# Kernel tuning notes

Hardware: AMD Instinct MI355X
Metric: run time of the kernel (lower is better)

The kernel has to match this reference:

```python
import jax, jax.numpy as jnp
import numpy as np

Q, A, R, S, K = 256, 28, 512, 256, 2  # n_quantize, n_aux, n_resch, n_skipch, kernel_size
DEPTH, REPEAT = 10, 3
L = DEPTH * REPEAT  # 30 layers
T = 8192


def setup_inputs() -> dict:
    key = jax.random.key(0)
    ks = jax.random.split(key, 24)
    w = lambda k, shape: jax.random.normal(k, shape, dtype=jnp.float32) * 0.05
    return {
        "x": jax.random.randint(ks[0], (1, T), 0, Q, dtype=jnp.int32),
        "h": jax.random.normal(ks[1], (1, A, T), dtype=jnp.float32),
        "Wc": w(ks[2], (R, Q, K)), "bc": w(ks[3], (R,)),
        "Wds": w(ks[4], (L, R, R, K)), "bds": w(ks[5], (L, R)),
        "Wdt": w(ks[6], (L, R, R, K)), "bdt": w(ks[7], (L, R)),
        "Was": w(ks[8], (L, R, A, 1)), "bas": w(ks[9], (L, R)),
        "Wat": w(ks[10], (L, R, A, 1)), "bat": w(ks[11], (L, R)),
        "Wsk": w(ks[12], (L, S, R, 1)), "bsk": w(ks[13], (L, S)),
        "Wr": w(ks[14], (L, R, R, 1)), "br": w(ks[15], (L, R)),
        "Wp1": w(ks[16], (S, S, 1)), "bp1": w(ks[17], (S,)),
        "Wp2": w(ks[18], (Q, S, 1)), "bp2": w(ks[19], (Q,)),
    }


def _cconv(z, w, b, d):
    # causal dilated conv: z [1,C,T], w [O,C,K] -> [1,O,T]
    pad = (w.shape[2] - 1) * d
    y = jax.lax.conv_general_dilated(
        z, w, window_strides=(1,), padding=[(pad, 0)], rhs_dilation=(d,),
        dimension_numbers=("NCH", "OIH", "NCH"))
    return y + b[None, :, None]


def reference(x, h, Wc, bc, Wds, bds, Wdt, bdt, Was, bas, Wat, bat,
              Wsk, bsk, Wr, br, Wp1, bp1, Wp2, bp2):
    dilations = [2 ** i for i in range(DEPTH)] * REPEAT
    oh = jax.nn.one_hot(x, Q, dtype=Wc.dtype).transpose(0, 2, 1)  # [1,Q,T]
    out = _cconv(oh, Wc, bc, 1)  # [1,R,T]
    skip_sum = jnp.zeros((1, S, oh.shape[2]), dtype=Wc.dtype)
    for l, d in enumerate(dilations):
        s = _cconv(out, Wds[l], bds[l], d) + _cconv(h, Was[l], bas[l], 1)
        t = _cconv(out, Wdt[l], bdt[l], d) + _cconv(h, Wat[l], bat[l], 1)
        g = jax.nn.sigmoid(s) * jnp.tanh(t)  # gated activation
        skip_sum = skip_sum + _cconv(g, Wsk[l], bsk[l], 1)
        out = _cconv(g, Wr[l], br[l], 1) + out  # residual
    o = jax.nn.relu(skip_sum)
    o = jax.nn.relu(_cconv(o, Wp1, bp1, 1))
    o = _cconv(o, Wp2, bp2, 1)  # [1,Q,T]
    return o[0].T  # [T,Q], matches squeeze(0).transpose(0,1)
```

## Files before the change

kernel.cpp:

```cpp
#include <hip/hip_runtime.h>
#include <hip/hip_bf16.h>
#include <math.h>
#include <stdint.h>

#define T_LEN 8192
#define RCH   512
#define SCH   256
#define QCH   256
#define ACH   28
#define NLAYER 30
#define KGATE 1088
#define KSR   512
#define KPOST 256

typedef _Float16 f16x8 __attribute__((ext_vector_type(8)));
typedef float    f32x4 __attribute__((ext_vector_type(4)));

#define SB0() __builtin_amdgcn_sched_barrier(0)

static __device__ __forceinline__ unsigned short f2h(float v) {
    _Float16 h = (_Float16)v;
    return *reinterpret_cast<unsigned short*>(&h);
}

static __device__ __forceinline__ float fsig(float x) {
    return __builtin_amdgcn_rcpf(1.f + __expf(-x));
}

#define G2L(SRC, DST) __builtin_amdgcn_global_load_lds(                        \
    (__attribute__((address_space(1))) void*)(const void*)(SRC),              \
    (__attribute__((address_space(3))) void*)(void*)(DST), 16, 0, 0)

__global__ void pack_gate_v(const float* __restrict__ Wds,
                            const float* __restrict__ Wdt,
                            const float* __restrict__ Was,
                            const float* __restrict__ Wat,
                            unsigned short* __restrict__ dst) {
    int l = blockIdx.y;
    int c = blockIdx.x * 256 + threadIdx.x;
    int tile = c >> 6, lane = c & 63;
    int mt = tile / 34, kt = tile % 34;
    int m  = mt * 16 + (lane & 15);
    int k0 = kt * 32 + (lane >> 4) * 8;
    int br = m & 1, ch = m >> 1;
    const float* Wd = (br ? Wdt : Wds) + (size_t)l * RCH * RCH * 2;
    const float* Wa = (br ? Wat : Was) + (size_t)l * RCH * ACH;
    unsigned short o[8];
    if (k0 < 512) {
        const float* base = Wd + ((size_t)ch * 512 + k0) * 2;
        #pragma unroll
        for (int q = 0; q < 4; ++q) {
            float4 v = *(const float4*)(base + q * 4);
            o[q * 2 + 0] = f2h(v.x);
            o[q * 2 + 1] = f2h(v.z);
        }
    } else if (k0 < 1024) {
        const float* base = Wd + ((size_t)ch * 512 + (k0 - 512)) * 2;
        #pragma unroll
        for (int q = 0; q < 4; ++q) {
            float4 v = *(const float4*)(base + q * 4);
            o[q * 2 + 0] = f2h(v.y);
            o[q * 2 + 1] = f2h(v.w);
        }
    } else {
        int a0 = k0 - 1024;
        #pragma unroll
        for (int i = 0; i < 8; ++i)
            o[i] = (a0 + i < ACH) ? f2h(Wa[(size_t)ch * ACH + a0 + i]) : (unsigned short)0;
    }
    *(uint4*)&dst[(size_t)l * 1024 * KGATE + (size_t)tile * 512 + lane * 8] = *(uint4*)o;
}

__global__ void pack_sr_v(const float* __restrict__ Wsk,
                          const float* __restrict__ Wr,
                          unsigned short* __restrict__ dst) {
    int l = blockIdx.y;
    int c = blockIdx.x * 256 + threadIdx.x;
    int tile = c >> 6, lane = c & 63;
    int mt = tile >> 4, kt = tile & 15;
    int m  = mt * 16 + (lane & 15);
    int k0 = kt * 32 + (lane >> 4) * 8;
    const float* row = (m < SCH) ? (Wsk + (size_t)l * SCH * RCH + (size_t)m * 512)
                                 : (Wr  + (size_t)l * RCH * RCH + (size_t)(m - SCH) * 512);
    float4 v0 = *(const float4*)(row + k0);
    float4 v1 = *(const float4*)(row + k0 + 4);
    unsigned short o[8] = { f2h(v0.x), f2h(v0.y), f2h(v0.z), f2h(v0.w),
                            f2h(v1.x), f2h(v1.y), f2h(v1.z), f2h(v1.w) };
    *(uint4*)&dst[(size_t)l * 768 * KSR + (size_t)tile * 512 + lane * 8] = *(uint4*)o;
}

__global__ void pack_post_v(const float* __restrict__ W,
                            unsigned short* __restrict__ dst) {
    int c = blockIdx.x * 256 + threadIdx.x;
    int tile = c >> 6, lane = c & 63;
    int mt = tile >> 3, kt = tile & 7;
    int m  = mt * 16 + (lane & 15);
    int k0 = kt * 32 + (lane >> 4) * 8;
    float4 v0 = *(const float4*)(W + (size_t)m * 256 + k0);
    float4 v1 = *(const float4*)(W + (size_t)m * 256 + k0 + 4);
    unsigned short o[8] = { f2h(v0.x), f2h(v0.y), f2h(v0.z), f2h(v0.w),
                            f2h(v1.x), f2h(v1.y), f2h(v1.z), f2h(v1.w) };
    *(uint4*)&dst[(size_t)tile * 512 + lane * 8] = *(uint4*)o;
}

__global__ void transpose_wc(const float* __restrict__ Wc,
                             float* __restrict__ WcT) {
    int idx = blockIdx.x * 256 + threadIdx.x;
    int r = idx >> 9;
    int qt = idx & 511;
    int q = qt >> 1, tap = qt & 1;
    WcT[(size_t)q * 1024 + tap * 512 + r] = Wc[(size_t)r * 512 + qt];
}

__global__ void embed_v(const int* __restrict__ x,
                        const float* __restrict__ WcT,
                        const float* __restrict__ bc,
                        float* __restrict__ out_tm,
                        unsigned short* __restrict__ outhf) {
    int idx = blockIdx.x * 256 + threadIdx.x;
    int t = idx >> 6, rc = (idx & 63) * 8;
    int x1 = x[t];
    const float* w1 = WcT + (size_t)x1 * 1024 + 512 + rc;
    float4 a = *(const float4*)w1;
    float4 b = *(const float4*)(w1 + 4);
    float4 c0 = *(const float4*)(bc + rc);
    float4 c1 = *(const float4*)(bc + rc + 4);
    a.x += c0.x; a.y += c0.y; a.z += c0.z; a.w += c0.w;
    b.x += c1.x; b.y += c1.y; b.z += c1.z; b.w += c1.w;
    if (t > 0) {
        const float* w0 = WcT + (size_t)x[t - 1] * 1024 + rc;
        float4 d0 = *(const float4*)w0;
        float4 d1 = *(const float4*)(w0 + 4);
        a.x += d0.x; a.y += d0.y; a.z += d0.z; a.w += d0.w;
        b.x += d1.x; b.y += d1.y; b.z += d1.z; b.w += d1.w;
    }
    size_t o = (size_t)t * 512 + rc;
    *(float4*)&out_tm[o] = a;
    *(float4*)&out_tm[o + 4] = b;
    unsigned short p[8] = { f2h(a.x), f2h(a.y), f2h(a.z), f2h(a.w),
                            f2h(b.x), f2h(b.y), f2h(b.z), f2h(b.w) };
    *(uint4*)&outhf[o + 512 * 512] = *(uint4*)p;
}

__global__ void packh_kernel(const float* __restrict__ h,
                             unsigned short* __restrict__ h_tm) {
    int idx = blockIdx.x * 256 + threadIdx.x;
    int t = idx >> 6, a = idx & 63;
    h_tm[idx] = f2h(a < ACH ? h[(size_t)a * T_LEN + t] : 0.f);
}

__global__ void reluconv_v(const float* __restrict__ skip,
                           unsigned short* __restrict__ dst) {
    int idx = (blockIdx.x * 256 + threadIdx.x) * 8;
    float4 v0 = *(const float4*)(skip + idx);
    float4 v1 = *(const float4*)(skip + idx + 4);
    unsigned short o[8] = { f2h(fmaxf(v0.x, 0.f)), f2h(fmaxf(v0.y, 0.f)),
                            f2h(fmaxf(v0.z, 0.f)), f2h(fmaxf(v0.w, 0.f)),
                            f2h(fmaxf(v1.x, 0.f)), f2h(fmaxf(v1.y, 0.f)),
                            f2h(fmaxf(v1.z, 0.f)), f2h(fmaxf(v1.w, 0.f)) };
    *(uint4*)&dst[idx] = *(uint4*)o;
}

template<int MODE, int KT64, int MB>
__global__ __launch_bounds__(256) void mfma_gemm(
    const unsigned short* __restrict__ Apk,
    const unsigned short* __restrict__ B0,
    const unsigned short* __restrict__ B2,
    const float* __restrict__ bias0, const float* __restrict__ bias1,
    const float* __restrict__ bias2, const float* __restrict__ bias3,
    float* __restrict__ O0, float* __restrict__ O1,
    unsigned short* __restrict__ OB, int dil)
{
    constexpr int KT32 = KT64 * 2;
    constexpr int NWG = MB * 64;
    constexpr int CPX = NWG / 8;

    __shared__ unsigned short Bsm[2][128 * 64];

    const int tid  = threadIdx.x;
    const int lane = tid & 63, wave = tid >> 6;
    const int wm = wave & 1, wn = wave >> 1;

    const int bid = blockIdx.x;
    const int swz = (bid & 7) * CPX + (bid >> 3);
    const int mb  = swz % MB;
    const int tb  = swz / MB;
    const int m0  = mb * 128;
    const int t0  = tb * 128;

    const int kc   = ((lane & 7) ^ (lane >> 3)) * 8;
    const int rsub = lane >> 3;

    const size_t mt0 = (size_t)(mb * 8) + wm * 4;

    f32x4 acc[4][4];
    #pragma unroll
    for (int a = 0; a < 4; ++a)
        #pragma unroll
        for (int b = 0; b < 4; ++b) acc[a][b] = (f32x4){0.f, 0.f, 0.f, 0.f};

    f16x8 afrA[4][2], afrB[4][2], bfr[4][2];

    auto stage_tile = [&](int kt, int buf) {
        const int kb = kt * 64;
        #pragma unroll
        for (int j = 0; j < 4; ++j) {
            const int row = wave * 32 + j * 8 + rsub;
            const int tg  = t0 + row;
            const unsigned short* src;
            if constexpr (MODE == 0) {
                if (kb < 512)
                    src = B0 + (size_t)(512 + tg - dil) * 512 + kb + kc;
                else if (kb < 1024)
                    src = B0 + (size_t)(512 + tg) * 512 + (kb - 512) + kc;
                else
                    src = B2 + (size_t)tg * 64 + kc;
            } else if constexpr (MODE == 1) {
                src = B0 + (size_t)tg * 512 + kb + kc;
            } else {
                src = B0 + (size_t)tg * 256 + kb + kc;
            }
            G2L(src, &Bsm[buf][(wave * 4 + j) * 512]);
        }
    };

    auto load_afr = [&](int kt, f16x8 (&dst)[4][2]) {
        #pragma unroll
        for (int mi = 0; mi < 4; ++mi)
            #pragma unroll
            for (int ks = 0; ks < 2; ++ks)
                dst[mi][ks] = *(const f16x8*)(Apk +
                    ((mt0 + mi) * KT32 + (size_t)(kt * 2 + ks)) * 512 + lane * 8);
    };

    auto load_bfr = [&](int buf) {
        #pragma unroll
        for (int ni = 0; ni < 4; ++ni)
            #pragma unroll
            for (int ks = 0; ks < 2; ++ks) {
                const int trow = wn * 64 + ni * 16 + (lane & 15);
                const int kch  = ks * 4 + (lane >> 4);
                const int sch  = kch ^ (lane & 7);
                bfr[ni][ks] = *(const f16x8*)&Bsm[buf][trow * 64 + sch * 8];
            }
    };

    auto do_mfma = [&](f16x8 (&A)[4][2]) {
        #pragma unroll
        for (int mi = 0; mi < 4; ++mi)
            #pragma unroll
            for (int ni = 0; ni < 4; ++ni) {
                acc[mi][ni] = __builtin_amdgcn_mfma_f32_16x16x32_f16(
                    A[mi][0], bfr[ni][0], acc[mi][ni], 0, 0, 0);
                acc[mi][ni] = __builtin_amdgcn_mfma_f32_16x16x32_f16(
                    A[mi][1], bfr[ni][1], acc[mi][ni], 0, 0, 0);
            }
    };

    stage_tile(0, 0);
    SB0();
    load_afr(0, afrA);
    SB0();
    asm volatile("s_waitcnt vmcnt(8)" ::: "memory");
    SB0();
    __builtin_amdgcn_s_barrier();

    #pragma unroll
    for (int kt = 0; kt < KT64; ++kt) {
        const int cur = kt & 1;
        if (kt + 1 < KT64) {
            stage_tile(kt + 1, cur ^ 1);
            SB0();
            if (cur) load_afr(kt + 1, afrA);
            else     load_afr(kt + 1, afrB);
            SB0();
        }
        load_bfr(cur);
        if (cur) do_mfma(afrB);
        else     do_mfma(afrA);
        if (kt + 1 < KT64) {
            SB0();
            asm volatile("s_waitcnt vmcnt(8) lgkmcnt(0)" ::: "memory");
            SB0();
            __builtin_amdgcn_s_barrier();
        }
    }

    const int rb0 = (lane >> 4) * 4;
    #pragma unroll
    for (int mi = 0; mi < 4; ++mi) {
        #pragma unroll
        for (int ni = 0; ni < 4; ++ni) {
            int m = m0 + wm * 64 + mi * 16 + rb0;
            int t = t0 + wn * 64 + ni * 16 + (lane & 15);
            f32x4 v = acc[mi][ni];
            if constexpr (MODE == 0) {
                int c0 = m >> 1;
                float s0 = v.x + bias0[c0]     + bias2[c0];
                float tv0 = v.y + bias1[c0]     + bias3[c0];
                float s1 = v.z + bias0[c0 + 1] + bias2[c0 + 1];
                float tv1 = v.w + bias1[c0 + 1] + bias3[c0 + 1];
                float g0 = fsig(s0) * (2.f * fsig(2.f * tv0) - 1.f);
                float g1 = fsig(s1) * (2.f * fsig(2.f * tv1) - 1.f);
                unsigned int p = (unsigned int)f2h(g0) | ((unsigned int)f2h(g1) << 16);
                *(unsigned int*)&OB[(size_t)t * 512 + c0] = p;
            } else if constexpr (MODE == 1) {
                if (m < SCH) {
                    float4* p = (float4*)&O0[(size_t)t * 256 + m];
                    float4 o = *p;
                    o.x += v.x + bias0[m + 0];
                    o.y += v.y + bias0[m + 1];
                    o.z += v.z + bias0[m + 2];
                    o.w += v.w + bias0[m + 3];
                    *p = o;
                } else {
                    int c = m - SCH;
                    float4* p = (float4*)&O1[(size_t)t * 512 + c];
                    float4 o = *p;
                    o.x += v.x + bias1[c + 0];
                    o.y += v.y + bias1[c + 1];
                    o.z += v.z + bias1[c + 2];
                    o.w += v.w + bias1[c + 3];
                    *p = o;
                    uint2 pk;
                    pk.x = (unsigned int)f2h(o.x) | ((unsigned int)f2h(o.y) << 16);
                    pk.y = (unsigned int)f2h(o.z) | ((unsigned int)f2h(o.w) << 16);
                    *(uint2*)&OB[(size_t)(512 + t) * 512 + c] = pk;
                }
            } else if constexpr (MODE == 2) {
                float o0 = fmaxf(v.x + bias0[m + 0], 0.f);
                float o1 = fmaxf(v.y + bias0[m + 1], 0.f);
                float o2 = fmaxf(v.z + bias0[m + 2], 0.f);
                float o3 = fmaxf(v.w + bias0[m + 3], 0.f);
                uint2 pk;
                pk.x = (unsigned int)f2h(o0) | ((unsigned int)f2h(o1) << 16);
                pk.y = (unsigned int)f2h(o2) | ((unsigned int)f2h(o3) << 16);
                *(uint2*)&OB[(size_t)t * 256 + m] = pk;
            } else {
                float4 o;
                o.x = v.x + bias0[m + 0];
                o.y = v.y + bias0[m + 1];
                o.z = v.z + bias0[m + 2];
                o.w = v.w + bias0[m + 3];
                *(float4*)&O0[(size_t)t * 256 + m] = o;
            }
        }
    }
}

extern "C" void kernel_launch(void* const* d_in, const int* in_sizes, int n_in,
                              void* d_out, int out_size, void* d_ws, size_t ws_size,
                              hipStream_t stream) {
    const int*   x   = (const int*)  d_in[0];
    const float* h   = (const float*)d_in[1];
    const float* Wc  = (const float*)d_in[2];
    const float* bc  = (const float*)d_in[3];
    const float* Wds = (const float*)d_in[4];
    const float* bds = (const float*)d_in[5];
    const float* Wdt = (const float*)d_in[6];
    const float* bdt = (const float*)d_in[7];
    const float* Was = (const float*)d_in[8];
    const float* bas = (const float*)d_in[9];
    const float* Wat = (const float*)d_in[10];
    const float* bat = (const float*)d_in[11];
    const float* Wsk = (const float*)d_in[12];
    const float* bsk = (const float*)d_in[13];
    const float* Wr  = (const float*)d_in[14];
    const float* br  = (const float*)d_in[15];
    const float* Wp1 = (const float*)d_in[16];
    const float* bp1 = (const float*)d_in[17];
    const float* Wp2 = (const float*)d_in[18];
    const float* bp2 = (const float*)d_in[19];
    float* dout = (float*)d_out;

    const size_t WG_EL  = (size_t)1024 * KGATE;
    const size_t WSR_EL = (size_t)768 * KSR;
    char* w = (char*)d_ws;
    float*          out_tm = (float*)w;               w += (size_t)T_LEN * 512 * 4;
    unsigned short* outhf  = (unsigned short*)w;      w += (size_t)(T_LEN + 512) * 512 * 2;
    unsigned short* g_tm   = (unsigned short*)w;      w += (size_t)T_LEN * 512 * 2;
    unsigned short* h_tm   = (unsigned short*)w;      w += (size_t)T_LEN * 64 * 2;
    unsigned short* skiphf = (unsigned short*)w;      w += (size_t)T_LEN * 256 * 2;
    unsigned short* o1hf   = (unsigned short*)w;      w += (size_t)T_LEN * 256 * 2;
    unsigned short* Wp1_pk = (unsigned short*)w;      w += (size_t)256 * 256 * 2;
    unsigned short* Wp2_pk = (unsigned short*)w;      w += (size_t)256 * 256 * 2;
    float*          WcT    = (float*)w;               w += (size_t)QCH * 2 * RCH * 4;
    unsigned short* Wg_pk  = (unsigned short*)w;
    size_t used_base = (size_t)((char*)Wg_pk - (char*)d_ws);
    size_t need_bulk = used_base + (WG_EL + WSR_EL) * NLAYER * 2;
    const bool bulk = ws_size >= need_bulk;
    unsigned short* Wsr_pk = Wg_pk + (bulk ? WG_EL * NLAYER : WG_EL);
    float* skip = dout;

    hipMemsetAsync(skip, 0, (size_t)T_LEN * 256 * 4, stream);
    hipMemsetAsync(outhf, 0, (size_t)512 * 512 * 2, stream);

    transpose_wc<<<1024, 256, 0, stream>>>(Wc, WcT);
    embed_v<<<(T_LEN * 64) / 256, 256, 0, stream>>>(x, WcT, bc, out_tm, outhf);
    packh_kernel<<<(T_LEN * 64) / 256, 256, 0, stream>>>(h, h_tm);
    pack_post_v<<<32, 256, 0, stream>>>(Wp1, Wp1_pk);
    pack_post_v<<<32, 256, 0, stream>>>(Wp2, Wp2_pk);

    if (bulk) {
        pack_gate_v<<<dim3(544, NLAYER), 256, 0, stream>>>(Wds, Wdt, Was, Wat, Wg_pk);
        pack_sr_v<<<dim3(192, NLAYER), 256, 0, stream>>>(Wsk, Wr, Wsr_pk);
    }

    for (int l = 0; l < NLAYER; ++l) {
        int dil = 1 << (l % 10);
        const unsigned short* wg;
        const unsigned short* wsr;
        if (bulk) {
            wg  = Wg_pk  + (size_t)l * WG_EL;
            wsr = Wsr_pk + (size_t)l * WSR_EL;
        } else {
            pack_gate_v<<<dim3(544, 1), 256, 0, stream>>>(
                Wds + (size_t)l * RCH * RCH * 2, Wdt + (size_t)l * RCH * RCH * 2,
                Was + (size_t)l * RCH * ACH, Wat + (size_t)l * RCH * ACH, Wg_pk);
            pack_sr_v<<<dim3(192, 1), 256, 0, stream>>>(
                Wsk + (size_t)l * SCH * RCH, Wr + (size_t)l * RCH * RCH, Wsr_pk);
            wg = Wg_pk; wsr = Wsr_pk;
        }
        mfma_gemm<0, KGATE / 64, 8><<<512, 256, 0, stream>>>(
            wg, outhf, h_tm,
            bds + (size_t)l * RCH, bdt + (size_t)l * RCH,
            bas + (size_t)l * RCH, bat + (size_t)l * RCH,
            nullptr, nullptr, g_tm, dil);
        mfma_gemm<1, KSR / 64, 6><<<384, 256, 0, stream>>>(
            wsr, g_tm, nullptr,
            bsk + (size_t)l * SCH, br + (size_t)l * RCH, nullptr, nullptr,
            skip, out_tm, outhf, 0);
    }

    reluconv_v<<<(T_LEN * 256 / 8) / 256, 256, 0, stream>>>(skip, skiphf);
    mfma_gemm<2, KPOST / 64, 2><<<128, 256, 0, stream>>>(
        Wp1_pk, skiphf, nullptr, bp1, nullptr, nullptr, nullptr,
        nullptr, nullptr, o1hf, 0);
    mfma_gemm<3, KPOST / 64, 2><<<128, 256, 0, stream>>>(
        Wp2_pk, o1hf, nullptr, bp2, nullptr, nullptr, nullptr,
        dout, nullptr, nullptr, 0);
}
```

Baseline: 1.545 ms.

## Use 512-thread 128x256 tiles with LDS-staged weights for per-layer GEMMs

Adds a new kernel for the gate and skip/residual GEMMs. It uses 512-thread workgroups covering 256 time steps instead of 128, and stages the packed weight (A) tiles through LDS instead of having each wave load them straight into registers. Weight tiles are now shared by 8 waves, and each A/B load is reused across a larger output tile, which cuts global/L2 traffic. The trade-offs are half as many workgroups (256 and 192), more LDS per block, and a full vmcnt(0) wait each k-step that reduces load/compute overlap. The post-processing GEMMs keep the old kernel under a slimmer signature.

```diff
diff --git a/kernel.cpp b/kernel.cpp
--- a/kernel.cpp
+++ b/kernel.cpp
@@ -162,7 +162,7 @@
 }
 
 template<int MODE, int KT64, int MB>
-__global__ __launch_bounds__(256) void mfma_gemm(
+__global__ __launch_bounds__(512) void mfma_gemm2(
     const unsigned short* __restrict__ Apk,
     const unsigned short* __restrict__ B0,
     const unsigned short* __restrict__ B2,
@@ -172,10 +172,11 @@
     unsigned short* __restrict__ OB, int dil)
 {
     constexpr int KT32 = KT64 * 2;
-    constexpr int NWG = MB * 64;
+    constexpr int NWG = MB * 32;
     constexpr int CPX = NWG / 8;
 
-    __shared__ unsigned short Bsm[2][128 * 64];
+    __shared__ unsigned short Asm[2][16 * 512];
+    __shared__ unsigned short Bsm[2][256 * 64];
 
     const int tid  = threadIdx.x;
     const int lane = tid & 63, wave = tid >> 6;
@@ -186,12 +187,10 @@
     const int mb  = swz % MB;
     const int tb  = swz / MB;
     const int m0  = mb * 128;
-    const int t0  = tb * 128;
+    const int t0  = tb * 256;
 
     const int kc   = ((lane & 7) ^ (lane >> 3)) * 8;
     const int rsub = lane >> 3;
-
-    const size_t mt0 = (size_t)(mb * 8) + wm * 4;
 
     f32x4 acc[4][4];
     #pragma unroll
@@ -199,9 +198,15 @@
         #pragma unroll
         for (int b = 0; b < 4; ++b) acc[a][b] = (f32x4){0.f, 0.f, 0.f, 0.f};
 
-    f16x8 afrA[4][2], afrB[4][2], bfr[4][2];
-
     auto stage_tile = [&](int kt, int buf) {
+        #pragma unroll
+        for (int c2 = 0; c2 < 2; ++c2) {
+            const int c  = wave * 2 + c2;
+            const int mt = c >> 1, ks = c & 1;
+            const unsigned short* src = Apk +
+                ((size_t)(mb * 8 + mt) * KT32 + (size_t)(kt * 2 + ks)) * 512 + lane * 8;
+            G2L(src, &Asm[buf][c * 512]);
+        }
         const int kb = kt * 64;
         #pragma unroll
         for (int j = 0; j < 4; ++j) {
@@ -215,25 +220,20 @@
                     src = B0 + (size_t)(512 + tg) * 512 + (kb - 512) + kc;
                 else
                     src = B2 + (size_t)tg * 64 + kc;
-            } else if constexpr (MODE == 1) {
+            } else {
                 src = B0 + (size_t)tg * 512 + kb + kc;
-            } else {
-                src = B0 + (size_t)tg * 256 + kb + kc;
-            }
-            G2L(src, &Bsm[buf][(wave * 4 + j) * 512]);
+            }
+            G2L(src, &Bsm[buf][(wave * 32 + j * 8) * 64]);
         }
     };
 
-    auto load_afr = [&](int kt, f16x8 (&dst)[4][2]) {
+    auto compute = [&](int buf) {
+        f16x8 afr[4][2], bfr[4][2];
         #pragma unroll
         for (int mi = 0; mi < 4; ++mi)
             #pragma unroll
             for (int ks = 0; ks < 2; ++ks)
-                dst[mi][ks] = *(const f16x8*)(Apk +
-                    ((mt0 + mi) * KT32 + (size_t)(kt * 2 + ks)) * 512 + lane * 8);
-    };
-
-    auto load_bfr = [&](int buf) {
+                afr[mi][ks] = *(const f16x8*)&Asm[buf][(((wm * 4 + mi) * 2 + ks) * 512) + lane * 8];
         #pragma unroll
         for (int ni = 0; ni < 4; ++ni)
             #pragma unroll
@@ -243,44 +243,33 @@
                 const int sch  = kch ^ (lane & 7);
                 bfr[ni][ks] = *(const f16x8*)&Bsm[buf][trow * 64 + sch * 8];
             }
-    };
-
-    auto do_mfma = [&](f16x8 (&A)[4][2]) {
         #pragma unroll
         for (int mi = 0; mi < 4; ++mi)
             #pragma unroll
             for (int ni = 0; ni < 4; ++ni) {
                 acc[mi][ni] = __builtin_amdgcn_mfma_f32_16x16x32_f16(
-                    A[mi][0], bfr[ni][0], acc[mi][ni], 0, 0, 0);
+                    afr[mi][0], bfr[ni][0], acc[mi][ni], 0, 0, 0);
                 acc[mi][ni] = __builtin_amdgcn_mfma_f32_16x16x32_f16(
-                    A[mi][1], bfr[ni][1], acc[mi][ni], 0, 0, 0);
+                    afr[mi][1], bfr[ni][1], acc[mi][ni], 0, 0, 0);
             }
     };
 
     stage_tile(0, 0);
     SB0();
-    load_afr(0, afrA);
-    SB0();
-    asm volatile("s_waitcnt vmcnt(8)" ::: "memory");
+    asm volatile("s_waitcnt vmcnt(0)" ::: "memory");
     SB0();
     __builtin_amdgcn_s_barrier();
 
     #pragma unroll
     for (int kt = 0; kt < KT64; ++kt) {
-        const int cur = kt & 1;
         if (kt + 1 < KT64) {
-            stage_tile(kt + 1, cur ^ 1);
-            SB0();
-            if (cur) load_afr(kt + 1, afrA);
-            else     load_afr(kt + 1, afrB);
-            SB0();
-        }
-        load_bfr(cur);
-        if (cur) do_mfma(afrB);
-        else     do_mfma(afrA);
+            stage_tile(kt + 1, (kt + 1) & 1);
+            SB0();
+        }
+        compute(kt & 1);
         if (kt + 1 < KT64) {
             SB0();
-            asm volatile("s_waitcnt vmcnt(8) lgkmcnt(0)" ::: "memory");
+            asm volatile("s_waitcnt vmcnt(0) lgkmcnt(0)" ::: "memory");
             SB0();
             __builtin_amdgcn_s_barrier();
         }
@@ -304,7 +293,7 @@
                 float g1 = fsig(s1) * (2.f * fsig(2.f * tv1) - 1.f);
                 unsigned int p = (unsigned int)f2h(g0) | ((unsigned int)f2h(g1) << 16);
                 *(unsigned int*)&OB[(size_t)t * 512 + c0] = p;
-            } else if constexpr (MODE == 1) {
+            } else {
                 if (m < SCH) {
                     float4* p = (float4*)&O0[(size_t)t * 256 + m];
                     float4 o = *p;
@@ -327,7 +316,124 @@
                     pk.y = (unsigned int)f2h(o.z) | ((unsigned int)f2h(o.w) << 16);
                     *(uint2*)&OB[(size_t)(512 + t) * 512 + c] = pk;
                 }
-            } else if constexpr (MODE == 2) {
+            }
+        }
+    }
+}
+
+template<int MODE, int KT64, int MB>
+__global__ __launch_bounds__(256) void mfma_gemm(
+    const unsigned short* __restrict__ Apk,
+    const unsigned short* __restrict__ B0,
+    const float* __restrict__ bias0,
+    float* __restrict__ O0, unsigned short* __restrict__ OB)
+{
+    constexpr int KT32 = KT64 * 2;
+    constexpr int NWG = MB * 64;
+    constexpr int CPX = NWG / 8;
+
+    __shared__ unsigned short Bsm[2][128 * 64];
+
+    const int tid  = threadIdx.x;
+    const int lane = tid & 63, wave = tid >> 6;
+    const int wm = wave & 1, wn = wave >> 1;
+
+    const int bid = blockIdx.x;
+    const int swz = (bid & 7) * CPX + (bid >> 3);
+    const int mb  = swz % MB;
+    const int tb  = swz / MB;
+    const int m0  = mb * 128;
+    const int t0  = tb * 128;
+
+    const int kc   = ((lane & 7) ^ (lane >> 3)) * 8;
+    const int rsub = lane >> 3;
+    const size_t mt0 = (size_t)(mb * 8) + wm * 4;
+
+    f32x4 acc[4][4];
+    #pragma unroll
+    for (int a = 0; a < 4; ++a)
+        #pragma unroll
+        for (int b = 0; b < 4; ++b) acc[a][b] = (f32x4){0.f, 0.f, 0.f, 0.f};
+
+    f16x8 afrA[4][2], afrB[4][2], bfr[4][2];
+
+    auto stage_tile = [&](int kt, int buf) {
+        #pragma unroll
+        for (int j = 0; j < 4; ++j) {
+            const int row = wave * 32 + j * 8 + rsub;
+            const unsigned short* src = B0 + (size_t)(t0 + row) * 256 + kt * 64 + kc;
+            G2L(src, &Bsm[buf][(wave * 4 + j) * 512]);
+        }
+    };
+    auto load_afr = [&](int kt, f16x8 (&dst)[4][2]) {
+        #pragma unroll
+        for (int mi = 0; mi < 4; ++mi)
+            #pragma unroll
+            for (int ks = 0; ks < 2; ++ks)
+                dst[mi][ks] = *(const f16x8*)(Apk +
+                    ((mt0 + mi) * KT32 + (size_t)(kt * 2 + ks)) * 512 + lane * 8);
+    };
+    auto load_bfr = [&](int buf) {
+        #pragma unroll
+        for (int ni = 0; ni < 4; ++ni)
+            #pragma unroll
+            for (int ks = 0; ks < 2; ++ks) {
+                const int trow = wn * 64 + ni * 16 + (lane & 15);
+                const int kch  = ks * 4 + (lane >> 4);
+                const int sch  = kch ^ (lane & 7);
+                bfr[ni][ks] = *(const f16x8*)&Bsm[buf][trow * 64 + sch * 8];
+            }
+    };
+    auto do_mfma = [&](f16x8 (&A)[4][2]) {
+        #pragma unroll
+        for (int mi = 0; mi < 4; ++mi)
+            #pragma unroll
+            for (int ni = 0; ni < 4; ++ni) {
+                acc[mi][ni] = __builtin_amdgcn_mfma_f32_16x16x32_f16(
+                    A[mi][0], bfr[ni][0], acc[mi][ni], 0, 0, 0);
+                acc[mi][ni] = __builtin_amdgcn_mfma_f32_16x16x32_f16(
+                    A[mi][1], bfr[ni][1], acc[mi][ni], 0, 0, 0);
+            }
+    };
+
+    stage_tile(0, 0);
+    SB0();
+    load_afr(0, afrA);
+    SB0();
+    asm volatile("s_waitcnt vmcnt(8)" ::: "memory");
+    SB0();
+    __builtin_amdgcn_s_barrier();
+
+    #pragma unroll
+    for (int kt = 0; kt < KT64; ++kt) {
+        const int cur = kt & 1;
+        if (kt + 1 < KT64) {
+            stage_tile(kt + 1, cur ^ 1);
+            SB0();
+            if (cur) load_afr(kt + 1, afrA);
+            else     load_afr(kt + 1, afrB);
+            SB0();
+        }
+        load_bfr(cur);
+        if (cur) do_mfma(afrB);
+        else     do_mfma(afrA);
+        if (kt + 1 < KT64) {
+            SB0();
+            asm volatile("s_waitcnt vmcnt(8) lgkmcnt(0)" ::: "memory");
+            SB0();
+            __builtin_amdgcn_s_barrier();
+        }
+    }
+
+    const int rb0 = (lane >> 4) * 4;
+    #pragma unroll
+    for (int mi = 0; mi < 4; ++mi) {
+        #pragma unroll
+        for (int ni = 0; ni < 4; ++ni) {
+            int m = m0 + wm * 64 + mi * 16 + rb0;
+            int t = t0 + wn * 64 + ni * 16 + (lane & 15);
+            f32x4 v = acc[mi][ni];
+            if constexpr (MODE == 2) {
                 float o0 = fmaxf(v.x + bias0[m + 0], 0.f);
                 float o1 = fmaxf(v.y + bias0[m + 1], 0.f);
                 float o2 = fmaxf(v.z + bias0[m + 2], 0.f);
@@ -421,12 +527,12 @@
                 Wsk + (size_t)l * SCH * RCH, Wr + (size_t)l * RCH * RCH, Wsr_pk);
             wg = Wg_pk; wsr = Wsr_pk;
         }
-        mfma_gemm<0, KGATE / 64, 8><<<512, 256, 0, stream>>>(
+        mfma_gemm2<0, KGATE / 64, 8><<<256, 512, 0, stream>>>(
             wg, outhf, h_tm,
             bds + (size_t)l * RCH, bdt + (size_t)l * RCH,
             bas + (size_t)l * RCH, bat + (size_t)l * RCH,
             nullptr, nullptr, g_tm, dil);
-        mfma_gemm<1, KSR / 64, 6><<<384, 256, 0, stream>>>(
+        mfma_gemm2<1, KSR / 64, 6><<<192, 512, 0, stream>>>(
             wsr, g_tm, nullptr,
             bsk + (size_t)l * SCH, br + (size_t)l * RCH, nullptr, nullptr,
             skip, out_tm, outhf, 0);
@@ -434,9 +540,7 @@
 
     reluconv_v<<<(T_LEN * 256 / 8) / 256, 256, 0, stream>>>(skip, skiphf);
     mfma_gemm<2, KPOST / 64, 2><<<128, 256, 0, stream>>>(
-        Wp1_pk, skiphf, nullptr, bp1, nullptr, nullptr, nullptr,
-        nullptr, nullptr, o1hf, 0);
+        Wp1_pk, skiphf, bp1, nullptr, o1hf);
     mfma_gemm<3, KPOST / 64, 2><<<128, 256, 0, stream>>>(
-        Wp2_pk, o1hf, nullptr, bp2, nullptr, nullptr, nullptr,
-        dout, nullptr, nullptr, 0);
-}
+        Wp2_pk, o1hf, bp2, dout, nullptr);
+}
```

Result: slower. 1.654 ms (+7.0%).
